# Kernel tuning notes

Measured on AMD Instinct MI355X. Metric: run time of the kernel, lower is better.

The kernel has to match this reference:

```python
import jax, jax.numpy as jnp
import numpy as np
import math

HIDDEN = 1024
HEADS = 16
HEAD_DIM = HIDDEN // HEADS
B, LQ, LK = 8, 16, 8192


def setup_inputs() -> dict:
    key = jax.random.key(0)
    ks = jax.random.split(key, 8)
    s = 1.0 / math.sqrt(HIDDEN)  # keep pre-softmax logits well-scaled
    return {
        "query": jax.random.normal(ks[0], (B, LQ, HIDDEN), jnp.float32),
        "key": jax.random.normal(ks[1], (B, LK, HIDDEN), jnp.float32),
        "value": jax.random.normal(ks[2], (B, LK, HIDDEN), jnp.float32),
        "Wq": jax.random.normal(ks[3], (HIDDEN, HIDDEN), jnp.float32) * s,
        "bq": jnp.zeros((HIDDEN,), jnp.float32),
        "Wk": jax.random.normal(ks[4], (HIDDEN, HIDDEN), jnp.float32) * s,
        "bk": jnp.zeros((HIDDEN,), jnp.float32),
        "Wv": jax.random.normal(ks[5], (HIDDEN, HIDDEN), jnp.float32) * s,
        "bv": jnp.zeros((HIDDEN,), jnp.float32),
        "Wo": jax.random.normal(ks[6], (HIDDEN, HIDDEN), jnp.float32) * s,
        "bo": jnp.zeros((HIDDEN,), jnp.float32),
    }


def reference(query, key, value, Wq, bq, Wk, bk, Wv, bv, Wo, bo):
    b, lq, _ = query.shape
    lk = key.shape[1]
    # Linear projections (torch Linear: x @ W.T + b), split into heads
    q = (query @ Wq.T + bq).reshape(b, lq, HEADS, HEAD_DIM)
    k = (key @ Wk.T + bk).reshape(b, lk, HEADS, HEAD_DIM)
    v = (value @ Wv.T + bv).reshape(b, lk, HEADS, HEAD_DIM)
    # scaled dot-product attention: scale query, QK^T, softmax, weighted sum
    scale = 1.0 / math.sqrt(HEAD_DIM)
    scores = jnp.einsum("bqhd,bkhd->bhqk", q * scale, k)  # [B,H,LQ,LK]
    probs = jax.nn.softmax(scores, axis=-1)
    attn = jnp.einsum("bhqk,bkhd->bqhd", probs, v).reshape(b, lq, HIDDEN)
    return attn @ Wo.T + bo
```

## Files before the change

### kernel.cpp

```cpp
#include <hip/hip_runtime.h>
#include <stdint.h>

#define NHEADS 16
#define LKK 8192
#define SPLIT 8
#define PSTR 72

typedef __attribute__((ext_vector_type(8))) short short8;
typedef __attribute__((ext_vector_type(4))) float f32x4;
typedef __attribute__((ext_vector_type(4))) unsigned short ushort4v;

__device__ __forceinline__ unsigned short f2bf(float f) {
  union { float f; unsigned u; } v; v.f = f;
  unsigned u = v.u;
  return (unsigned short)((u + 0x7fffu + ((u >> 16) & 1u)) >> 16);
}

__device__ __forceinline__ void async_ld16(const void* g, void* l) {
  __builtin_amdgcn_global_load_lds(
      (const __attribute__((address_space(1))) unsigned int*)g,
      (__attribute__((address_space(3))) unsigned int*)l, 16, 0, 0);
}

__global__ __launch_bounds__(256) void cvt2(const float* __restrict__ a,
                                            const float* __restrict__ b,
                                            unsigned short* __restrict__ oa,
                                            unsigned short* __restrict__ ob) {
  const float* s = blockIdx.y ? b : a;
  unsigned short* d = blockIdx.y ? ob : oa;
  const size_t i = ((size_t)blockIdx.x * 256 + threadIdx.x) * 4;
  float4 v = *(const float4*)(s + i);
  ushort4v o = {f2bf(v.x), f2bf(v.y), f2bf(v.z), f2bf(v.w)};
  *(ushort4v*)(d + i) = o;
}

template <int MODE, int LOG2ROWS>
__global__ __launch_bounds__(256) void gemm_nt(
    const unsigned short* __restrict__ A, const unsigned short* __restrict__ Bw,
    const float* __restrict__ bias, float scale, void* __restrict__ outp) {
  __shared__ unsigned short As[128 * 32];
  __shared__ unsigned short Bs[128 * 32];

  const int tid = threadIdx.x;
  const int wave = tid >> 6, lane = tid & 63;
  const int quad = lane >> 4, l16 = lane & 15;
  const int wr = wave >> 1, wc = wave & 1;

  const int gx = gridDim.x;
  const int nwg = gx * 8;
  int id = blockIdx.y * gx + blockIdx.x;
  const int cpx = nwg >> 3;
  id = (id & 7) * cpx + (id >> 3);
  const int bm = id >> 3, bn = id & 7;

  f32x4 acc[4][4] = {};

  const int srow = lane >> 2;
  const int sseg = lane & 3;
  const unsigned short* Ag =
      A + (size_t)(bm * 128 + wave * 32 + srow) * 1024 + sseg * 8;
  const unsigned short* Bg =
      Bw + (size_t)(bn * 128 + wave * 32 + srow) * 1024 + sseg * 8;
  unsigned short* AsW = As + wave * 32 * 32;
  unsigned short* BsW = Bs + wave * 32 * 32;

  for (int kk = 0; kk < 32; ++kk) {
    const int k0 = kk * 32;
    __syncthreads();
    async_ld16(Ag + k0, AsW);
    async_ld16(Ag + 16 * 1024 + k0, AsW + 16 * 32);
    async_ld16(Bg + k0, BsW);
    async_ld16(Bg + 16 * 1024 + k0, BsW + 16 * 32);
    __syncthreads();

    short8 af[4], bf[4];
#pragma unroll
    for (int i = 0; i < 4; ++i)
      af[i] = *(const short8*)(As + (wr * 64 + i * 16 + l16) * 32 + quad * 8);
#pragma unroll
    for (int j = 0; j < 4; ++j)
      bf[j] = *(const short8*)(Bs + (wc * 64 + j * 16 + l16) * 32 + quad * 8);
#pragma unroll
    for (int i = 0; i < 4; ++i)
#pragma unroll
      for (int j = 0; j < 4; ++j)
        acc[i][j] =
            __builtin_amdgcn_mfma_f32_16x16x32_bf16(af[i], bf[j], acc[i][j], 0, 0, 0);
  }

  float bvals[4];
#pragma unroll
  for (int j = 0; j < 4; ++j) bvals[j] = bias[bn * 128 + wc * 64 + j * 16 + l16];

#pragma unroll
  for (int i = 0; i < 4; ++i) {
    const int gm0 = bm * 128 + wr * 64 + i * 16 + quad * 4;
#pragma unroll
    for (int j = 0; j < 4; ++j) {
      const int gn = bn * 128 + wc * 64 + j * 16 + l16;
      float vals[4];
#pragma unroll
      for (int r = 0; r < 4; ++r) vals[r] = (acc[i][j][r] + bvals[j]) * scale;
      if constexpr (MODE == 0) {
        float* O = (float*)outp;
#pragma unroll
        for (int r = 0; r < 4; ++r) O[(size_t)(gm0 + r) * 1024 + gn] = vals[r];
      } else if constexpr (MODE == 1) {
        unsigned short* O = (unsigned short*)outp;
        const int h = gn >> 6, d = gn & 63;
#pragma unroll
        for (int r = 0; r < 4; ++r) {
          const int m = gm0 + r;
          const int bb = m >> LOG2ROWS;
          const int x = m & ((1 << LOG2ROWS) - 1);
          O[((((size_t)(bb * 16 + h)) << LOG2ROWS) + x) * 64 + d] = f2bf(vals[r]);
        }
      } else {
        unsigned short* O = (unsigned short*)outp;
        const int h = gn >> 6, d = gn & 63;
        const int bb = gm0 >> LOG2ROWS;
        const int x = gm0 & ((1 << LOG2ROWS) - 1);
        ushort4v pk = {f2bf(vals[0]), f2bf(vals[1]), f2bf(vals[2]), f2bf(vals[3])};
        *(ushort4v*)(O + ((((size_t)(bb * 16 + h)) * 64 + d) << LOG2ROWS) + x) = pk;
      }
    }
  }
}

__global__ __launch_bounds__(256) void attn_split(
    const unsigned short* __restrict__ q_hd,
    const unsigned short* __restrict__ k_hd,
    const unsigned short* __restrict__ v_t,
    float* __restrict__ part_O,
    float* __restrict__ part_ml)
{
  __shared__ unsigned short p_lds[4][16 * PSTR];
  __shared__ float o_lds[4][16][64];
  __shared__ float ml_lds[4][2][16];

  const int h = blockIdx.x, b = blockIdx.y, sp = blockIdx.z;
  const int tid = threadIdx.x, wave = tid >> 6, lane = tid & 63;
  const int quad = lane >> 4, l16 = lane & 15;
  const size_t bh = (size_t)(b * NHEADS + h);
  const float LOG2E = 1.44269504088896f;

  const unsigned short* qb = q_hd + bh * (16 * 64) + l16 * 64 + quad * 8;
  short8 aq0 = *(const short8*)(qb);
  short8 aq1 = *(const short8*)(qb + 32);

  const unsigned short* kb_base = k_hd + bh * ((size_t)LKK * 64);
  const unsigned short* vb_base = v_t + bh * ((size_t)64 * LKK);

  float ms[4], ls[4];
  f32x4 o[4] = {};
#pragma unroll
  for (int r = 0; r < 4; ++r) { ms[r] = -3.0e38f; ls[r] = 0.f; }

  unsigned short* pw = &p_lds[wave][0];
  const int jbase = sp * (LKK / SPLIT) + wave * (LKK / SPLIT / 4);

  for (int c = 0; c < (LKK / SPLIT / 4) / 64; ++c) {
    const int j0 = jbase + c * 64;
    short8 kf[4][2];
#pragma unroll
    for (int jt = 0; jt < 4; ++jt)
#pragma unroll
      for (int dh = 0; dh < 2; ++dh)
        kf[jt][dh] = *(const short8*)(kb_base + (size_t)(j0 + jt * 16 + l16) * 64 +
                                      dh * 32 + quad * 8);
    f32x4 s[4];
#pragma unroll
    for (int jt = 0; jt < 4; ++jt) {
      f32x4 z = {};
      z = __builtin_amdgcn_mfma_f32_16x16x32_bf16(aq0, kf[jt][0], z, 0, 0, 0);
      z = __builtin_amdgcn_mfma_f32_16x16x32_bf16(aq1, kf[jt][1], z, 0, 0, 0);
      s[jt] = z;
    }
    float p[4][4], alpha[4];
#pragma unroll
    for (int r = 0; r < 4; ++r) {
      float v = fmaxf(fmaxf(s[0][r], s[1][r]), fmaxf(s[2][r], s[3][r]));
      v = fmaxf(v, __shfl_xor(v, 1));
      v = fmaxf(v, __shfl_xor(v, 2));
      v = fmaxf(v, __shfl_xor(v, 4));
      v = fmaxf(v, __shfl_xor(v, 8));
      const float mn = fmaxf(ms[r], v);
      alpha[r] = __builtin_amdgcn_exp2f((ms[r] - mn) * LOG2E);
      float rs = 0.f;
#pragma unroll
      for (int jt = 0; jt < 4; ++jt) {
        p[jt][r] = __builtin_amdgcn_exp2f((s[jt][r] - mn) * LOG2E);
        rs += p[jt][r];
      }
      ls[r] = ls[r] * alpha[r] + rs;
      ms[r] = mn;
    }
#pragma unroll
    for (int dt = 0; dt < 4; ++dt) {
      f32x4 t = o[dt];
      t[0] *= alpha[0]; t[1] *= alpha[1]; t[2] *= alpha[2]; t[3] *= alpha[3];
      o[dt] = t;
    }
#pragma unroll
    for (int r = 0; r < 4; ++r)
#pragma unroll
      for (int jt = 0; jt < 4; ++jt)
        pw[(quad * 4 + r) * PSTR + jt * 16 + l16] = f2bf(p[jt][r]);
    short8 pa[2];
#pragma unroll
    for (int kt = 0; kt < 2; ++kt)
      pa[kt] = *(const short8*)(pw + l16 * PSTR + kt * 32 + quad * 8);
#pragma unroll
    for (int dt = 0; dt < 4; ++dt)
#pragma unroll
      for (int kt = 0; kt < 2; ++kt) {
        short8 vb = *(const short8*)(vb_base + (size_t)(dt * 16 + l16) * LKK + j0 +
                                     kt * 32 + quad * 8);
        o[dt] = __builtin_amdgcn_mfma_f32_16x16x32_bf16(pa[kt], vb, o[dt], 0, 0, 0);
      }
  }

#pragma unroll
  for (int r = 0; r < 4; ++r) {
    ls[r] += __shfl_xor(ls[r], 1);
    ls[r] += __shfl_xor(ls[r], 2);
    ls[r] += __shfl_xor(ls[r], 4);
    ls[r] += __shfl_xor(ls[r], 8);
  }

#pragma unroll
  for (int dt = 0; dt < 4; ++dt)
#pragma unroll
    for (int r = 0; r < 4; ++r) o_lds[wave][quad * 4 + r][dt * 16 + l16] = o[dt][r];
  if (l16 == 0) {
#pragma unroll
    for (int r = 0; r < 4; ++r) {
      ml_lds[wave][0][quad * 4 + r] = ms[r];
      ml_lds[wave][1][quad * 4 + r] = ls[r];
    }
  }
  __syncthreads();

  const int q = tid >> 4;
  const int d0 = (tid & 15) * 4;
  float mstar = ml_lds[0][0][q];
#pragma unroll
  for (int w = 1; w < 4; ++w) mstar = fmaxf(mstar, ml_lds[w][0][q]);
  float lstar = 0.f, ov[4] = {0.f, 0.f, 0.f, 0.f};
#pragma unroll
  for (int w = 0; w < 4; ++w) {
    const float sc = __builtin_amdgcn_exp2f((ml_lds[w][0][q] - mstar) * LOG2E);
    lstar += ml_lds[w][1][q] * sc;
#pragma unroll
    for (int e = 0; e < 4; ++e) ov[e] += o_lds[w][q][d0 + e] * sc;
  }
  const size_t base = (bh * SPLIT + sp);
#pragma unroll
  for (int e = 0; e < 4; ++e) part_O[base * 1024 + q * 64 + d0 + e] = ov[e];
  if (d0 == 0) {
    part_ml[base * 32 + q] = mstar;
    part_ml[base * 32 + 16 + q] = lstar;
  }
}

__global__ __launch_bounds__(256) void attn_merge(const float* __restrict__ part_O,
                                                  const float* __restrict__ part_ml,
                                                  unsigned short* __restrict__ attn_b) {
  const int bh = blockIdx.x;
  const int b = bh >> 4, h = bh & 15;
  const int q = threadIdx.x >> 4;
  const int d0 = (threadIdx.x & 15) * 4;
  const float LOG2E = 1.44269504088896f;

  float mstar = -3.0e38f;
#pragma unroll
  for (int s = 0; s < SPLIT; ++s)
    mstar = fmaxf(mstar, part_ml[((size_t)bh * SPLIT + s) * 32 + q]);
  float lsum = 0.f, ov[4] = {0.f, 0.f, 0.f, 0.f};
#pragma unroll
  for (int s = 0; s < SPLIT; ++s) {
    const size_t base = (size_t)bh * SPLIT + s;
    const float sc = __builtin_amdgcn_exp2f((part_ml[base * 32 + q] - mstar) * LOG2E);
    lsum += part_ml[base * 32 + 16 + q] * sc;
#pragma unroll
    for (int e = 0; e < 4; ++e) ov[e] += part_O[base * 1024 + q * 64 + d0 + e] * sc;
  }
  const float inv = 1.0f / lsum;
  ushort4v pk = {f2bf(ov[0] * inv), f2bf(ov[1] * inv), f2bf(ov[2] * inv),
                 f2bf(ov[3] * inv)};
  *(ushort4v*)(attn_b + (size_t)(b * 16 + q) * 1024 + h * 64 + d0) = pk;
}

extern "C" void kernel_launch(void* const* d_in, const int* in_sizes, int n_in,
                              void* d_out, int out_size, void* d_ws, size_t ws_size,
                              hipStream_t stream) {
  const float* query = (const float*)d_in[0];
  const float* key = (const float*)d_in[1];
  const float* value = (const float*)d_in[2];
  const float* Wq = (const float*)d_in[3];
  const float* bq = (const float*)d_in[4];
  const float* Wk = (const float*)d_in[5];
  const float* bk = (const float*)d_in[6];
  const float* Wv = (const float*)d_in[7];
  const float* bv = (const float*)d_in[8];
  const float* Wo = (const float*)d_in[9];
  const float* bo = (const float*)d_in[10];
  float* out = (float*)d_out;

  char* ws = (char*)d_ws;
  size_t off = 0;
  auto alloc = [&](size_t bytes) {
    void* p = ws + off;
    off += (bytes + 255) & ~(size_t)255;
    return p;
  };
  unsigned short* Wq_b = (unsigned short*)alloc((size_t)1024 * 1024 * 2);
  unsigned short* Wk_b = (unsigned short*)alloc((size_t)1024 * 1024 * 2);
  unsigned short* Wv_b = (unsigned short*)alloc((size_t)1024 * 1024 * 2);
  unsigned short* Wo_b = (unsigned short*)alloc((size_t)1024 * 1024 * 2);
  unsigned short* query_b = (unsigned short*)alloc((size_t)128 * 1024 * 2);
  unsigned short* q_hd = (unsigned short*)alloc((size_t)128 * 1024 * 2);
  unsigned short* attn_b = (unsigned short*)alloc((size_t)128 * 1024 * 2);
  float* part_O = (float*)alloc((size_t)128 * SPLIT * 16 * 64 * 4);
  float* part_ml = (float*)alloc((size_t)128 * SPLIT * 32 * 4);
  unsigned short* k_hd = (unsigned short*)alloc((size_t)128 * LKK * 64 * 2);
  unsigned short* v_t = (unsigned short*)alloc((size_t)128 * LKK * 64 * 2);
  unsigned short* stage = (unsigned short*)alloc((size_t)65536 * 1024 * 2);

  cvt2<<<dim3(1024, 2), 256, 0, stream>>>(Wq, Wk, Wq_b, Wk_b);
  cvt2<<<dim3(1024, 2), 256, 0, stream>>>(Wv, Wo, Wv_b, Wo_b);
  cvt2<<<dim3(128, 1), 256, 0, stream>>>(query, nullptr, query_b, nullptr);

  gemm_nt<1, 4><<<dim3(1, 8), 256, 0, stream>>>(query_b, Wq_b, bq, 0.125f, q_hd);

  cvt2<<<dim3(65536, 1), 256, 0, stream>>>(key, nullptr, stage, nullptr);
  gemm_nt<1, 13><<<dim3(512, 8), 256, 0, stream>>>(stage, Wk_b, bk, 1.0f, k_hd);

  cvt2<<<dim3(65536, 1), 256, 0, stream>>>(value, nullptr, stage, nullptr);
  gemm_nt<2, 13><<<dim3(512, 8), 256, 0, stream>>>(stage, Wv_b, bv, 1.0f, v_t);

  attn_split<<<dim3(16, 8, SPLIT), 256, 0, stream>>>(q_hd, k_hd, v_t, part_O, part_ml);
  attn_merge<<<128, 256, 0, stream>>>(part_O, part_ml, attn_b);

  gemm_nt<0, 0><<<dim3(1, 8), 256, 0, stream>>>(attn_b, Wo_b, bo, 1.0f, out);
}
```

Baseline: 1.058 ms.

## Add 256x256 double-buffered swizzled GEMM for K and V projections

Replaces the 128x128 single-buffered GEMM used for the large K and V projections with a new 512-thread kernel. It uses 256x256 tiles with K-step 64, double-buffered async global-to-LDS loads, an XOR-swizzled LDS layout to avoid bank conflicts, and interleaved prefetch with MFMA phases under raised wave priority. The aim is to raise arithmetic intensity and overlap memory with compute in the dominant GEMMs. It uses 128KB of LDS and many accumulator registers, so only one block fits per CU, and the hand-placed waitcnt ordering is fragile.

```diff
diff --git a/kernel.cpp b/kernel.cpp
--- a/kernel.cpp
+++ b/kernel.cpp
@@ -34,6 +34,139 @@
   *(ushort4v*)(d + i) = o;
 }
 
+#define MM(MI, A0, A1)                                                        \
+  {                                                                           \
+    _Pragma("unroll") for (int n = 0; n < 4; ++n) {                           \
+      acc[MI][n] = __builtin_amdgcn_mfma_f32_16x16x32_bf16(A0, bf[n][0],      \
+                                                           acc[MI][n], 0, 0, 0); \
+      acc[MI][n] = __builtin_amdgcn_mfma_f32_16x16x32_bf16(A1, bf[n][1],      \
+                                                           acc[MI][n], 0, 0, 0); \
+    }                                                                         \
+  }
+
+template <int MODE>
+__global__ __launch_bounds__(512) void gemm_big(
+    const unsigned short* __restrict__ A, const unsigned short* __restrict__ Bw,
+    const float* __restrict__ bias, unsigned short* __restrict__ O) {
+  __shared__ __align__(16) unsigned short lds[2][2][256 * 64];
+
+  const int tid = threadIdx.x;
+  const int wave = tid >> 6, lane = tid & 63;
+  const int quad = lane >> 4, l16 = lane & 15, l7 = l16 & 7;
+  const int wr = wave >> 2, wc = wave & 3;
+
+  int id = blockIdx.x;
+  id = (id & 7) * 128 + (id >> 3);
+  const int bm = id >> 2, bn = id & 3;
+  const int row0 = bm * 256, col0 = bn * 256;
+
+  const int lr = tid >> 3;
+  const int seg_src = (tid & 7) ^ (lr & 7);
+  const unsigned short* Asrc = A + (size_t)(row0 + lr) * 1024 + seg_src * 8;
+  const unsigned short* Bsrc = Bw + (size_t)(col0 + lr) * 1024 + seg_src * 8;
+
+  f32x4 acc[8][4] = {};
+  short8 bf[4][2];
+
+#define STG(MAT, NXT, KT, Q)                                                  \
+  async_ld16(((MAT) ? Bsrc : Asrc) + (size_t)(Q) * 64 * 1024 + (KT) * 64,     \
+             &lds[NXT][MAT][(Q) * 4096 + wave * 512])
+#define BARX() asm volatile("s_barrier" ::: "memory")
+#define RD_A(MI, KS)                                                          \
+  (*(const short8*)(ldsA + (wr * 128 + (MI) * 16 + l16) * 64 +                \
+                    ((((KS) * 4 + quad) ^ l7) * 8)))
+#define RD_B(NN, KS)                                                          \
+  (*(const short8*)(ldsB + (wc * 64 + (NN) * 16 + l16) * 64 +                 \
+                    ((((KS) * 4 + quad) ^ l7) * 8)))
+
+  STG(1, 0, 0, 0); STG(1, 0, 0, 1); STG(1, 0, 0, 2); STG(1, 0, 0, 3);
+  STG(0, 0, 0, 0); STG(0, 0, 0, 2); STG(0, 0, 0, 1); STG(0, 0, 0, 3);
+  asm volatile("s_waitcnt vmcnt(2)" ::: "memory");
+  BARX();
+
+#pragma unroll 2
+  for (int kt = 0; kt < 16; ++kt) {
+    const int cur = kt & 1, nxt = cur ^ 1;
+    const bool pf = kt < 15;
+    const unsigned short* ldsA = &lds[cur][0][0];
+    const unsigned short* ldsB = &lds[cur][1][0];
+
+    {
+#pragma unroll
+      for (int n = 0; n < 4; ++n) { bf[n][0] = RD_B(n, 0); bf[n][1] = RD_B(n, 1); }
+      short8 a0 = RD_A(0, 0), a1 = RD_A(0, 1), a2 = RD_A(1, 0), a3 = RD_A(1, 1);
+      if (pf) { STG(1, nxt, kt + 1, 0); STG(1, nxt, kt + 1, 1); }
+      BARX();
+      __builtin_amdgcn_s_setprio(1);
+      MM(0, a0, a1); MM(1, a2, a3);
+      __builtin_amdgcn_s_setprio(0);
+      BARX();
+    }
+    {
+      short8 a0 = RD_A(2, 0), a1 = RD_A(2, 1), a2 = RD_A(3, 0), a3 = RD_A(3, 1);
+      if (pf) { STG(1, nxt, kt + 1, 2); STG(1, nxt, kt + 1, 3); }
+      BARX();
+      __builtin_amdgcn_s_setprio(1);
+      MM(2, a0, a1); MM(3, a2, a3);
+      __builtin_amdgcn_s_setprio(0);
+      if (pf) asm volatile("s_waitcnt vmcnt(4)" ::: "memory");
+      else    asm volatile("s_waitcnt vmcnt(0)" ::: "memory");
+      BARX();
+    }
+    {
+      short8 a0 = RD_A(4, 0), a1 = RD_A(4, 1), a2 = RD_A(5, 0), a3 = RD_A(5, 1);
+      if (pf) { STG(0, nxt, kt + 1, 0); STG(0, nxt, kt + 1, 2); }
+      BARX();
+      __builtin_amdgcn_s_setprio(1);
+      MM(4, a0, a1); MM(5, a2, a3);
+      __builtin_amdgcn_s_setprio(0);
+      BARX();
+    }
+    {
+      short8 a0 = RD_A(6, 0), a1 = RD_A(6, 1), a2 = RD_A(7, 0), a3 = RD_A(7, 1);
+      if (pf) { STG(0, nxt, kt + 1, 1); STG(0, nxt, kt + 1, 3); }
+      BARX();
+      __builtin_amdgcn_s_setprio(1);
+      MM(6, a0, a1); MM(7, a2, a3);
+      __builtin_amdgcn_s_setprio(0);
+      if (pf) asm volatile("s_waitcnt vmcnt(2)" ::: "memory");
+      BARX();
+    }
+  }
+#undef RD_A
+#undef RD_B
+#undef STG
+
+  float bvals[4];
+#pragma unroll
+  for (int n = 0; n < 4; ++n) bvals[n] = bias[col0 + wc * 64 + n * 16 + l16];
+
+#pragma unroll
+  for (int mi = 0; mi < 8; ++mi) {
+    const int gm0 = row0 + wr * 128 + mi * 16 + quad * 4;
+#pragma unroll
+    for (int n = 0; n < 4; ++n) {
+      const int gn = col0 + wc * 64 + n * 16 + l16;
+      const int h = gn >> 6, d = gn & 63;
+      float vals[4];
+#pragma unroll
+      for (int r = 0; r < 4; ++r) vals[r] = acc[mi][n][r] + bvals[n];
+      if constexpr (MODE == 1) {
+#pragma unroll
+        for (int r = 0; r < 4; ++r) {
+          const int m = gm0 + r;
+          const int bb = m >> 13, x = m & 8191;
+          O[((((size_t)(bb * 16 + h)) << 13) + x) * 64 + d] = f2bf(vals[r]);
+        }
+      } else {
+        const int bb = gm0 >> 13, x = gm0 & 8191;
+        ushort4v pk = {f2bf(vals[0]), f2bf(vals[1]), f2bf(vals[2]), f2bf(vals[3])};
+        *(ushort4v*)(O + ((((size_t)(bb * 16 + h)) * 64 + d) << 13) + x) = pk;
+      }
+    }
+  }
+}
+
 template <int MODE, int LOG2ROWS>
 __global__ __launch_bounds__(256) void gemm_nt(
     const unsigned short* __restrict__ A, const unsigned short* __restrict__ Bw,
@@ -73,19 +206,19 @@
     async_ld16(Bg + 16 * 1024 + k0, BsW + 16 * 32);
     __syncthreads();
 
-    short8 af[4], bf[4];
+    short8 af[4], bfr[4];
 #pragma unroll
     for (int i = 0; i < 4; ++i)
       af[i] = *(const short8*)(As + (wr * 64 + i * 16 + l16) * 32 + quad * 8);
 #pragma unroll
     for (int j = 0; j < 4; ++j)
-      bf[j] = *(const short8*)(Bs + (wc * 64 + j * 16 + l16) * 32 + quad * 8);
+      bfr[j] = *(const short8*)(Bs + (wc * 64 + j * 16 + l16) * 32 + quad * 8);
 #pragma unroll
     for (int i = 0; i < 4; ++i)
 #pragma unroll
       for (int j = 0; j < 4; ++j)
         acc[i][j] =
-            __builtin_amdgcn_mfma_f32_16x16x32_bf16(af[i], bf[j], acc[i][j], 0, 0, 0);
+            __builtin_amdgcn_mfma_f32_16x16x32_bf16(af[i], bfr[j], acc[i][j], 0, 0, 0);
   }
 
   float bvals[4];
@@ -102,26 +235,26 @@
 #pragma unroll
       for (int r = 0; r < 4; ++r) vals[r] = (acc[i][j][r] + bvals[j]) * scale;
       if constexpr (MODE == 0) {
-        float* O = (float*)outp;
-#pragma unroll
-        for (int r = 0; r < 4; ++r) O[(size_t)(gm0 + r) * 1024 + gn] = vals[r];
+        float* Of = (float*)outp;
+#pragma unroll
+        for (int r = 0; r < 4; ++r) Of[(size_t)(gm0 + r) * 1024 + gn] = vals[r];
       } else if constexpr (MODE == 1) {
-        unsigned short* O = (unsigned short*)outp;
+        unsigned short* Ou = (unsigned short*)outp;
         const int h = gn >> 6, d = gn & 63;
 #pragma unroll
         for (int r = 0; r < 4; ++r) {
           const int m = gm0 + r;
           const int bb = m >> LOG2ROWS;
           const int x = m & ((1 << LOG2ROWS) - 1);
-          O[((((size_t)(bb * 16 + h)) << LOG2ROWS) + x) * 64 + d] = f2bf(vals[r]);
+          Ou[((((size_t)(bb * 16 + h)) << LOG2ROWS) + x) * 64 + d] = f2bf(vals[r]);
         }
       } else {
-        unsigned short* O = (unsigned short*)outp;
+        unsigned short* Ou = (unsigned short*)outp;
         const int h = gn >> 6, d = gn & 63;
         const int bb = gm0 >> LOG2ROWS;
         const int x = gm0 & ((1 << LOG2ROWS) - 1);
         ushort4v pk = {f2bf(vals[0]), f2bf(vals[1]), f2bf(vals[2]), f2bf(vals[3])};
-        *(ushort4v*)(O + ((((size_t)(bb * 16 + h)) * 64 + d) << LOG2ROWS) + x) = pk;
+        *(ushort4v*)(Ou + ((((size_t)(bb * 16 + h)) * 64 + d) << LOG2ROWS) + x) = pk;
       }
     }
   }
@@ -334,10 +467,10 @@
   gemm_nt<1, 4><<<dim3(1, 8), 256, 0, stream>>>(query_b, Wq_b, bq, 0.125f, q_hd);
 
   cvt2<<<dim3(65536, 1), 256, 0, stream>>>(key, nullptr, stage, nullptr);
-  gemm_nt<1, 13><<<dim3(512, 8), 256, 0, stream>>>(stage, Wk_b, bk, 1.0f, k_hd);
+  gemm_big<1><<<dim3(1024), 512, 0, stream>>>(stage, Wk_b, bk, k_hd);
 
   cvt2<<<dim3(65536, 1), 256, 0, stream>>>(value, nullptr, stage, nullptr);
-  gemm_nt<2, 13><<<dim3(512, 8), 256, 0, stream>>>(stage, Wv_b, bv, 1.0f, v_t);
+  gemm_big<2><<<dim3(1024), 512, 0, stream>>>(stage, Wv_b, bv, v_t);
 
   attn_split<<<dim3(16, 8, SPLIT), 256, 0, stream>>>(q_hd, k_hd, v_t, part_O, part_ml);
   attn_merge<<<128, 256, 0, stream>>>(part_O, part_ml, attn_b);
```

Measured after the change: 937.3 us. -11.4%, faster.
